# Kernel tuning notes

Measured on AMD Instinct MI355X. Metric: run time of the kernel, lower is better.

The kernel has to match this reference:

```python
import jax, jax.numpy as jnp
import numpy as np

N_NODES = 50000
N_EDGES = 800000
N_GRAPHS = 512
VOCAB = 128
HID = 64
NCLS = 5


def _seg_mean(vals, ids, num_segments):
    s = jax.ops.segment_sum(vals, ids, num_segments=num_segments)
    cnt = jax.ops.segment_sum(jnp.ones((vals.shape[0],), vals.dtype), ids, num_segments=num_segments)
    return s / jnp.maximum(cnt, 1.0)[:, None]


def sage_conv(x, src, dst, W_l, b_l, W_r):
    # PyG SAGEConv (mean aggr): out = lin_l(mean_{j in N(i)} x_j) + lin_r(x_i)
    agg = _seg_mean(x[src], dst, x.shape[0])          # [N, H] gather + scatter-mean
    return agg @ W_l.T + b_l + x @ W_r.T


def setup_inputs() -> dict:
    key = jax.random.key(0)
    ks = jax.random.split(key, 10)
    scale = 1.0 / np.sqrt(HID)
    x_tokens = jax.random.randint(ks[0], (N_NODES,), 0, VOCAB)
    edge_index = jax.random.randint(ks[1], (2, N_EDGES), 0, N_NODES)
    batch = jnp.sort(jax.random.randint(ks[2], (N_NODES,), 0, N_GRAPHS))
    return {
        "x_tokens": x_tokens,
        "edge_index": edge_index,
        "batch": batch,
        "embed": jax.random.normal(ks[3], (VOCAB, HID), jnp.float32),
        "W1l": jax.random.normal(ks[4], (HID, HID), jnp.float32) * scale,
        "b1l": jnp.zeros((HID,), jnp.float32),
        "W1r": jax.random.normal(ks[5], (HID, HID), jnp.float32) * scale,
        "W2l": jax.random.normal(ks[6], (HID, HID), jnp.float32) * scale,
        "b2l": jnp.zeros((HID,), jnp.float32),
        "W2r": jax.random.normal(ks[7], (HID, HID), jnp.float32) * scale,
        "Wlin": jax.random.normal(ks[8], (NCLS, HID), jnp.float32) * scale,
        "blin": jnp.zeros((NCLS,), jnp.float32),
    }


def reference(x_tokens, edge_index, batch, embed, W1l, b1l, W1r, W2l, b2l, W2r, Wlin, blin):
    src, dst = edge_index[0], edge_index[1]
    x = embed[x_tokens]                                  # [N, H] embedding lookup
    x = jax.nn.relu(sage_conv(x, src, dst, W1l, b1l, W1r))
    x = jax.nn.relu(sage_conv(x, src, dst, W2l, b2l, W2r))
    g = _seg_mean(x, batch, N_GRAPHS)                    # global_mean_pool -> [G, H]
    return g @ Wlin.T + blin                             # [G, num_classes]
```

## Files before the change

kernel.cpp:

```cpp
#include <hip/hip_runtime.h>

#define N_NODES  50000
#define N_EDGES  800000
#define N_GRAPHS 512
#define HID      64
#define NCLS     5
#define NB       64
#define EST      36

typedef __attribute__((ext_vector_type(8))) short bf16x8;
typedef __attribute__((ext_vector_type(4))) float f32x4;

__device__ inline unsigned short f2bf(float f) {
    unsigned int u = __builtin_bit_cast(unsigned int, f);
    unsigned int r = (u + 0x7FFFu + ((u >> 16) & 1u)) >> 16;
    return (unsigned short)r;
}
__device__ inline unsigned int packbf(float a, float b) {
    return (unsigned int)f2bf(a) | ((unsigned int)f2bf(b) << 16);
}
__device__ inline float bf2f(unsigned int u16) {
    unsigned int t = u16 << 16;
    return __builtin_bit_cast(float, t);
}

#define EBUF_T (128 * 32)
#define PW_T   (64 * 64)
#define PREP_T (EBUF_T + N_NODES + 2 * PW_T)
__global__ void k_prep(const float* __restrict__ embed, unsigned int* __restrict__ ebufg,
                       const int* __restrict__ batch,
                       int* __restrict__ pos_start, int* __restrict__ pos_end,
                       const float* __restrict__ W1l, const float* __restrict__ W1r,
                       unsigned int* __restrict__ wb1,
                       const float* __restrict__ W2l, const float* __restrict__ W2r,
                       unsigned int* __restrict__ wb2) {
    int gid = blockIdx.x * blockDim.x + threadIdx.x;
    if (gid < EBUF_T) {
        int t = gid >> 5, c = gid & 31;
        float2 v = ((const float2*)(embed + (long)t * HID))[c];
        ebufg[gid] = packbf(v.x, v.y);
        return;
    }
    gid -= EBUF_T;
    if (gid < N_NODES) {
        int n = gid;
        int b = batch[n];
        if (n == 0 || batch[n - 1] != b) pos_start[b] = n;
        if (n == N_NODES - 1 || batch[n + 1] != b) pos_end[b] = n + 1;
        return;
    }
    gid -= N_NODES;
    if (gid < 2 * PW_T) {
        const float* Wl = (gid < PW_T) ? W1l : W2l;
        const float* Wr = (gid < PW_T) ? W1r : W2r;
        unsigned int* wb = (gid < PW_T) ? wb1 : wb2;
        int i = (gid < PW_T) ? gid : gid - PW_T;
        int h = i >> 6, c = i & 63;
        float2 v = (c < 32) ? ((const float2*)(Wl + (long)h * HID))[c]
                            : ((const float2*)(Wr + (long)h * HID))[c - 32];
        wb[i] = packbf(v.x, v.y);
    }
}

__global__ void k_fill(const int* __restrict__ src, const int* __restrict__ dst,
                       const int* __restrict__ tok,
                       int* __restrict__ cnt, unsigned int* __restrict__ bucket) {
    int e = blockIdx.x * blockDim.x + threadIdx.x;
    if (e >= N_EDGES) return;
    int s = src[e], d = dst[e];
    unsigned int t = (unsigned int)tok[s];
    int pos = atomicAdd(&cnt[d], 1);
    if (pos < NB) bucket[(long)d * NB + pos] = (unsigned int)s | (t << 16);
}

__global__ __launch_bounds__(256) void k_agg1(
    const int* __restrict__ cnt, const unsigned int* __restrict__ bucket,
    const unsigned int* __restrict__ ebufg, unsigned int* __restrict__ aggb) {
    __shared__ unsigned int elds[128 * EST];
    const int tid = threadIdx.x;
    for (int i = tid; i < EBUF_T; i += 256) {
        int t = i >> 5, c = i & 31;
        elds[t * EST + c] = ebufg[i];
    }
    __syncthreads();

    int n    = (blockIdx.x * 256 + tid) >> 6;
    int lane = tid & 63;
    int q    = lane & 7;
    int e8   = lane >> 3;
    int deg  = cnt[n];
    int m    = min(deg, NB);
    unsigned int v = (lane < m) ? bucket[(long)n * NB + lane] : 0u;
    float f0 = 0, f1 = 0, f2 = 0, f3 = 0, f4 = 0, f5 = 0, f6 = 0, f7 = 0;
#pragma unroll
    for (int g = 0; g < 8; ++g) {
        int j = g * 8 + e8;
        unsigned int vv = __shfl(v, j, 64);
        if (j < m) {
            int tk = (int)(vv >> 16);
            uint4 w = *((const uint4*)(elds + tk * EST + q * 4));
            f0 += bf2f(w.x & 0xffff); f1 += bf2f(w.x >> 16);
            f2 += bf2f(w.y & 0xffff); f3 += bf2f(w.y >> 16);
            f4 += bf2f(w.z & 0xffff); f5 += bf2f(w.z >> 16);
            f6 += bf2f(w.w & 0xffff); f7 += bf2f(w.w >> 16);
        }
    }
#pragma unroll
    for (int o = 8; o < 64; o <<= 1) {
        f0 += __shfl_xor(f0, o, 64); f1 += __shfl_xor(f1, o, 64);
        f2 += __shfl_xor(f2, o, 64); f3 += __shfl_xor(f3, o, 64);
        f4 += __shfl_xor(f4, o, 64); f5 += __shfl_xor(f5, o, 64);
        f6 += __shfl_xor(f6, o, 64); f7 += __shfl_xor(f7, o, 64);
    }
    if (e8 == 0) {
        float inv = 1.0f / (float)max(deg, 1);
        uint4 o;
        o.x = packbf(f0 * inv, f1 * inv);
        o.y = packbf(f2 * inv, f3 * inv);
        o.z = packbf(f4 * inv, f5 * inv);
        o.w = packbf(f6 * inv, f7 * inv);
        *((uint4*)(aggb + (long)n * 32) + q) = o;
    }
}

__global__ __launch_bounds__(256) void k_agg2(
    const int* __restrict__ cnt, const unsigned int* __restrict__ bucket,
    const unsigned int* __restrict__ xb, unsigned int* __restrict__ aggb) {
    const int tid = threadIdx.x;
    int n    = (blockIdx.x * 256 + tid) >> 6;
    int lane = tid & 63;
    int q    = lane & 7;
    int e8   = lane >> 3;
    int deg  = cnt[n];
    int m    = min(deg, NB);
    unsigned int v = (lane < m) ? bucket[(long)n * NB + lane] : 0u;
    float f0 = 0, f1 = 0, f2 = 0, f3 = 0, f4 = 0, f5 = 0, f6 = 0, f7 = 0;
#pragma unroll
    for (int g = 0; g < 8; ++g) {
        int j = g * 8 + e8;
        unsigned int vv = __shfl(v, j, 64);
        if (j < m) {
            int s = (int)(vv & 0xffffu);
            uint4 w = *((const uint4*)(xb + (long)s * 32) + q);
            f0 += bf2f(w.x & 0xffff); f1 += bf2f(w.x >> 16);
            f2 += bf2f(w.y & 0xffff); f3 += bf2f(w.y >> 16);
            f4 += bf2f(w.z & 0xffff); f5 += bf2f(w.z >> 16);
            f6 += bf2f(w.w & 0xffff); f7 += bf2f(w.w >> 16);
        }
    }
#pragma unroll
    for (int o = 8; o < 64; o <<= 1) {
        f0 += __shfl_xor(f0, o, 64); f1 += __shfl_xor(f1, o, 64);
        f2 += __shfl_xor(f2, o, 64); f3 += __shfl_xor(f3, o, 64);
        f4 += __shfl_xor(f4, o, 64); f5 += __shfl_xor(f5, o, 64);
        f6 += __shfl_xor(f6, o, 64); f7 += __shfl_xor(f7, o, 64);
    }
    if (e8 == 0) {
        float inv = 1.0f / (float)max(deg, 1);
        uint4 o;
        o.x = packbf(f0 * inv, f1 * inv);
        o.y = packbf(f2 * inv, f3 * inv);
        o.z = packbf(f4 * inv, f5 * inv);
        o.w = packbf(f6 * inv, f7 * inv);
        *((uint4*)(aggb + (long)n * 32) + q) = o;
    }
}

__global__ __launch_bounds__(256) void k_transform(
    const unsigned int* __restrict__ aggb, const unsigned int* __restrict__ xsrc,
    const int* __restrict__ tok,
    const unsigned int* __restrict__ wb, const float* __restrict__ bl,
    unsigned short* __restrict__ xoutb)
{
    const int tid  = threadIdx.x;
    const int lane = tid & 63;
    const int w    = tid >> 6;
    const int nb   = blockIdx.x * 64 + w * 16;
    const int m    = lane & 15;
    const int quad = lane >> 4;

    int row  = nb + m;
    int rowc = min(row, N_NODES - 1);
    const unsigned int* selfp = tok ? (xsrc + (long)tok[rowc] * 32)
                                    : (xsrc + (long)rowc * 32);

    bf16x8 afr[4];
    afr[0] = *(const bf16x8*)(aggb + (long)rowc * 32 + quad * 4);
    afr[1] = *(const bf16x8*)(aggb + (long)rowc * 32 + 16 + quad * 4);
    afr[2] = *(const bf16x8*)(selfp + quad * 4);
    afr[3] = *(const bf16x8*)(selfp + 16 + quad * 4);

    f32x4 acc[4];
#pragma unroll
    for (int t = 0; t < 4; ++t) {
        acc[t] = (f32x4){0.f, 0.f, 0.f, 0.f};
#pragma unroll
        for (int kst = 0; kst < 4; ++kst) {
            bf16x8 bfr = *(const bf16x8*)(wb + (t * 16 + m) * 64 + kst * 16 + quad * 4);
            acc[t] = __builtin_amdgcn_mfma_f32_16x16x32_bf16(bfr, afr[kst], acc[t], 0, 0, 0);
        }
    }

    int node = nb + m;
    if (node < N_NODES) {
#pragma unroll
        for (int t = 0; t < 4; ++t) {
            int hb = t * 16 + quad * 4;
            float4 bb = *(const float4*)(bl + hb);
            ushort4 o;
            o.x = f2bf(fmaxf(acc[t][0] + bb.x, 0.f));
            o.y = f2bf(fmaxf(acc[t][1] + bb.y, 0.f));
            o.z = f2bf(fmaxf(acc[t][2] + bb.z, 0.f));
            o.w = f2bf(fmaxf(acc[t][3] + bb.w, 0.f));
            *(ushort4*)(xoutb + (long)node * HID + hb) = o;
        }
    }
}

__global__ __launch_bounds__(64) void k_pool(
    const unsigned int* __restrict__ x2b,
    const int* __restrict__ pos_start, const int* __restrict__ pos_end,
    const float* __restrict__ Wlin, const float* __restrict__ blin,
    float* __restrict__ out)
{
    int g    = blockIdx.x;
    int lane = threadIdx.x;
    int q    = lane & 7;
    int slot = lane >> 3;
    int s = pos_start[g], e = pos_end[g];
    float f0 = 0, f1 = 0, f2 = 0, f3 = 0, f4 = 0, f5 = 0, f6 = 0, f7 = 0;
    for (int n = s + slot; n < e; n += 8) {
        uint4 v = *((const uint4*)(x2b + (long)n * 32) + q);
        f0 += bf2f(v.x & 0xffff); f1 += bf2f(v.x >> 16);
        f2 += bf2f(v.y & 0xffff); f3 += bf2f(v.y >> 16);
        f4 += bf2f(v.z & 0xffff); f5 += bf2f(v.z >> 16);
        f6 += bf2f(v.w & 0xffff); f7 += bf2f(v.w >> 16);
    }
#pragma unroll
    for (int o = 8; o < 64; o <<= 1) {
        f0 += __shfl_xor(f0, o, 64); f1 += __shfl_xor(f1, o, 64);
        f2 += __shfl_xor(f2, o, 64); f3 += __shfl_xor(f3, o, 64);
        f4 += __shfl_xor(f4, o, 64); f5 += __shfl_xor(f5, o, 64);
        f6 += __shfl_xor(f6, o, 64); f7 += __shfl_xor(f7, o, 64);
    }
    float inv = 1.0f / (float)max(e - s, 1);
    f0 *= inv; f1 *= inv; f2 *= inv; f3 *= inv;
    f4 *= inv; f5 *= inv; f6 *= inv; f7 *= inv;
#pragma unroll
    for (int c = 0; c < NCLS; ++c) {
        const float* wr = Wlin + c * HID + q * 8;
        float p = f0 * wr[0] + f1 * wr[1] + f2 * wr[2] + f3 * wr[3] +
                  f4 * wr[4] + f5 * wr[5] + f6 * wr[6] + f7 * wr[7];
        p += __shfl_xor(p, 1, 64);
        p += __shfl_xor(p, 2, 64);
        p += __shfl_xor(p, 4, 64);
        if (lane == 0) out[g * NCLS + c] = p + blin[c];
    }
}

extern "C" void kernel_launch(void* const* d_in, const int* in_sizes, int n_in,
                              void* d_out, int out_size, void* d_ws, size_t ws_size,
                              hipStream_t stream) {
    const int*   tok   = (const int*)d_in[0];
    const int*   eidx  = (const int*)d_in[1];
    const int*   batch = (const int*)d_in[2];
    const float* embed = (const float*)d_in[3];
    const float* W1l   = (const float*)d_in[4];
    const float* b1l   = (const float*)d_in[5];
    const float* W1r   = (const float*)d_in[6];
    const float* W2l   = (const float*)d_in[7];
    const float* b2l   = (const float*)d_in[8];
    const float* W2r   = (const float*)d_in[9];
    const float* Wlin  = (const float*)d_in[10];
    const float* blin  = (const float*)d_in[11];
    float* out = (float*)d_out;

    const int* src = eidx;
    const int* dst = eidx + N_EDGES;

    char* wsp = (char*)d_ws;
    size_t off = 0;
    auto alloc = [&](size_t bytes) -> void* {
        void* p = wsp + off;
        off = (off + bytes + 255) & ~(size_t)255;
        return p;
    };
    int*   cnt     = (int*)  alloc((size_t)N_NODES * 4);
    int*   pstart  = (int*)  alloc((size_t)N_GRAPHS * 4);
    int*   pend    = (int*)  alloc((size_t)N_GRAPHS * 4);
    unsigned int* bucket = (unsigned int*)alloc((size_t)N_NODES * NB * 4);
    unsigned int* aggb   = (unsigned int*)alloc((size_t)N_NODES * 32 * 4);
    unsigned int* x1b    = (unsigned int*)alloc((size_t)N_NODES * 32 * 4);
    unsigned int* x2b    = (unsigned int*)alloc((size_t)N_NODES * 32 * 4);
    unsigned int* ebufg  = (unsigned int*)alloc((size_t)128 * 32 * 4);
    unsigned int* wb1    = (unsigned int*)alloc((size_t)64 * 64 * 4);
    unsigned int* wb2    = (unsigned int*)alloc((size_t)64 * 64 * 4);

    hipMemsetAsync(cnt, 0, (char*)pend - (char*)cnt + (size_t)N_GRAPHS * 4, stream);

    k_prep<<<(PREP_T + 255) / 256, 256, 0, stream>>>(
        embed, ebufg, batch, pstart, pend, W1l, W1r, wb1, W2l, W2r, wb2);

    k_fill<<<(N_EDGES + 255) / 256, 256, 0, stream>>>(src, dst, tok, cnt, bucket);

    const int ABLK = (N_NODES * 64) / 256;
    const int TBLK = (N_NODES + 63) / 64;
    k_agg1<<<ABLK, 256, 0, stream>>>(cnt, bucket, ebufg, aggb);
    k_transform<<<TBLK, 256, 0, stream>>>(aggb, ebufg, tok, wb1, b1l,
                                          (unsigned short*)x1b);
    k_agg2<<<ABLK, 256, 0, stream>>>(cnt, bucket, x1b, aggb);
    k_transform<<<TBLK, 256, 0, stream>>>(aggb, x1b, nullptr, wb2, b2l,
                                          (unsigned short*)x2b);

    k_pool<<<N_GRAPHS, 64, 0, stream>>>(x2b, pstart, pend, Wlin, blin, out);
}
```

Before: 212.6 us.

## Pre-pack edges in prep and partition bucket fill by destination residue

The token lookup and src/dst packing move into the prep kernel, which writes an 8-byte packed edge array. The fill kernel then launches 8 groups of blocks, each scanning all edges but handling only destinations whose index mod 8 matches the group. The aim is to localize atomic and scatter traffic into the per-node buckets and improve cache or XCD locality. In exchange, the edge array is read eight times, and an extra 6.4MB intermediate is written and read back.

```diff
diff --git a/kernel.cpp b/kernel.cpp
--- a/kernel.cpp
+++ b/kernel.cpp
@@ -7,6 +7,7 @@
 #define NCLS     5
 #define NB       64
 #define EST      36
+#define FILL_GB  128
 
 typedef __attribute__((ext_vector_type(8))) short bf16x8;
 typedef __attribute__((ext_vector_type(4))) float f32x4;
@@ -26,14 +27,17 @@
 
 #define EBUF_T (128 * 32)
 #define PW_T   (64 * 64)
-#define PREP_T (EBUF_T + N_NODES + 2 * PW_T)
-__global__ void k_prep(const float* __restrict__ embed, unsigned int* __restrict__ ebufg,
-                       const int* __restrict__ batch,
-                       int* __restrict__ pos_start, int* __restrict__ pos_end,
-                       const float* __restrict__ W1l, const float* __restrict__ W1r,
-                       unsigned int* __restrict__ wb1,
-                       const float* __restrict__ W2l, const float* __restrict__ W2r,
-                       unsigned int* __restrict__ wb2) {
+#define PREP_T (EBUF_T + N_NODES + 2 * PW_T + N_EDGES)
+__global__ void k_prep(
+    const float* __restrict__ embed, unsigned int* __restrict__ ebufg,
+    const int* __restrict__ batch,
+    int* __restrict__ pos_start, int* __restrict__ pos_end,
+    const float* __restrict__ W1l, const float* __restrict__ W1r,
+    unsigned int* __restrict__ wb1,
+    const float* __restrict__ W2l, const float* __restrict__ W2r,
+    unsigned int* __restrict__ wb2,
+    const int* __restrict__ src, const int* __restrict__ dst,
+    const int* __restrict__ tok, uint2* __restrict__ epack) {
     int gid = blockIdx.x * blockDim.x + threadIdx.x;
     if (gid < EBUF_T) {
         int t = gid >> 5, c = gid & 31;
@@ -59,18 +63,29 @@
         float2 v = (c < 32) ? ((const float2*)(Wl + (long)h * HID))[c]
                             : ((const float2*)(Wr + (long)h * HID))[c - 32];
         wb[i] = packbf(v.x, v.y);
-    }
-}
-
-__global__ void k_fill(const int* __restrict__ src, const int* __restrict__ dst,
-                       const int* __restrict__ tok,
-                       int* __restrict__ cnt, unsigned int* __restrict__ bucket) {
-    int e = blockIdx.x * blockDim.x + threadIdx.x;
-    if (e >= N_EDGES) return;
-    int s = src[e], d = dst[e];
-    unsigned int t = (unsigned int)tok[s];
-    int pos = atomicAdd(&cnt[d], 1);
-    if (pos < NB) bucket[(long)d * NB + pos] = (unsigned int)s | (t << 16);
+        return;
+    }
+    gid -= 2 * PW_T;
+    if (gid < N_EDGES) {
+        int s = src[gid];
+        unsigned int t = (unsigned int)tok[s];
+        epack[gid] = make_uint2((unsigned int)s | (t << 16), (unsigned int)dst[gid]);
+    }
+}
+
+__global__ __launch_bounds__(256) void k_fill(
+    const uint2* __restrict__ epack, int* __restrict__ cnt,
+    unsigned int* __restrict__ bucket) {
+    const int x  = blockIdx.x & 7;
+    const int bs = blockIdx.x >> 3;
+    for (int e = bs * 256 + threadIdx.x; e < N_EDGES; e += 256 * FILL_GB) {
+        uint2 v = epack[e];
+        int d = (int)v.y;
+        if ((d & 7) == x) {
+            int pos = atomicAdd(&cnt[d], 1);
+            if (pos < NB) bucket[(long)d * NB + pos] = v.x;
+        }
+    }
 }
 
 __global__ __launch_bounds__(256) void k_agg1(
@@ -289,6 +304,7 @@
     int*   pstart  = (int*)  alloc((size_t)N_GRAPHS * 4);
     int*   pend    = (int*)  alloc((size_t)N_GRAPHS * 4);
     unsigned int* bucket = (unsigned int*)alloc((size_t)N_NODES * NB * 4);
+    uint2* epack         = (uint2*)alloc((size_t)N_EDGES * 8);
     unsigned int* aggb   = (unsigned int*)alloc((size_t)N_NODES * 32 * 4);
     unsigned int* x1b    = (unsigned int*)alloc((size_t)N_NODES * 32 * 4);
     unsigned int* x2b    = (unsigned int*)alloc((size_t)N_NODES * 32 * 4);
@@ -299,9 +315,10 @@
     hipMemsetAsync(cnt, 0, (char*)pend - (char*)cnt + (size_t)N_GRAPHS * 4, stream);
 
     k_prep<<<(PREP_T + 255) / 256, 256, 0, stream>>>(
-        embed, ebufg, batch, pstart, pend, W1l, W1r, wb1, W2l, W2r, wb2);
-
-    k_fill<<<(N_EDGES + 255) / 256, 256, 0, stream>>>(src, dst, tok, cnt, bucket);
+        embed, ebufg, batch, pstart, pend, W1l, W1r, wb1, W2l, W2r, wb2,
+        src, dst, tok, epack);
+
+    k_fill<<<8 * FILL_GB, 256, 0, stream>>>(epack, cnt, bucket);
 
     const int ABLK = (N_NODES * 64) / 256;
     const int TBLK = (N_NODES + 63) / 64;
```

Result: no change. 215.8 us (+1.5%).

## Fuse neighbor aggregation and linear transform into one per-layer kernel

Applied to the files above, without the earlier changes.

Each SAGE layer now runs as a single kernel: 1024-thread blocks aggregate the neighbor means for 64 nodes into a shared-memory tile together with the self features, then run the MFMA transform straight from LDS. This removes the global aggb round-trip and two kernel launches. The cost is larger blocks that need a full-block barrier, and each wave does four nodes in sequence, which lowers occupancy and leaves less latency hiding for the gathers.

```diff
diff --git a/kernel.cpp b/kernel.cpp
--- a/kernel.cpp
+++ b/kernel.cpp
@@ -7,6 +7,7 @@
 #define NCLS     5
 #define NB       64
 #define EST      36
+#define AST      68
 
 typedef __attribute__((ext_vector_type(8))) short bf16x8;
 typedef __attribute__((ext_vector_type(4))) float f32x4;
@@ -27,13 +28,14 @@
 #define EBUF_T (128 * 32)
 #define PW_T   (64 * 64)
 #define PREP_T (EBUF_T + N_NODES + 2 * PW_T)
-__global__ void k_prep(const float* __restrict__ embed, unsigned int* __restrict__ ebufg,
-                       const int* __restrict__ batch,
-                       int* __restrict__ pos_start, int* __restrict__ pos_end,
-                       const float* __restrict__ W1l, const float* __restrict__ W1r,
-                       unsigned int* __restrict__ wb1,
-                       const float* __restrict__ W2l, const float* __restrict__ W2r,
-                       unsigned int* __restrict__ wb2) {
+__global__ void k_prep(
+    const float* __restrict__ embed, unsigned int* __restrict__ ebufg,
+    const int* __restrict__ batch,
+    int* __restrict__ pos_start, int* __restrict__ pos_end,
+    const float* __restrict__ W1l, const float* __restrict__ W1r,
+    unsigned int* __restrict__ wb1,
+    const float* __restrict__ W2l, const float* __restrict__ W2r,
+    unsigned int* __restrict__ wb2) {
     int gid = blockIdx.x * blockDim.x + threadIdx.x;
     if (gid < EBUF_T) {
         int t = gid >> 5, c = gid & 31;
@@ -73,147 +75,106 @@
     if (pos < NB) bucket[(long)d * NB + pos] = (unsigned int)s | (t << 16);
 }
 
-__global__ __launch_bounds__(256) void k_agg1(
+template <bool L1>
+__global__ __launch_bounds__(1024) void k_layer(
     const int* __restrict__ cnt, const unsigned int* __restrict__ bucket,
-    const unsigned int* __restrict__ ebufg, unsigned int* __restrict__ aggb) {
-    __shared__ unsigned int elds[128 * EST];
-    const int tid = threadIdx.x;
-    for (int i = tid; i < EBUF_T; i += 256) {
-        int t = i >> 5, c = i & 31;
-        elds[t * EST + c] = ebufg[i];
-    }
-    __syncthreads();
-
-    int n    = (blockIdx.x * 256 + tid) >> 6;
-    int lane = tid & 63;
-    int q    = lane & 7;
-    int e8   = lane >> 3;
-    int deg  = cnt[n];
-    int m    = min(deg, NB);
-    unsigned int v = (lane < m) ? bucket[(long)n * NB + lane] : 0u;
-    float f0 = 0, f1 = 0, f2 = 0, f3 = 0, f4 = 0, f5 = 0, f6 = 0, f7 = 0;
-#pragma unroll
-    for (int g = 0; g < 8; ++g) {
-        int j = g * 8 + e8;
-        unsigned int vv = __shfl(v, j, 64);
-        if (j < m) {
-            int tk = (int)(vv >> 16);
-            uint4 w = *((const uint4*)(elds + tk * EST + q * 4));
-            f0 += bf2f(w.x & 0xffff); f1 += bf2f(w.x >> 16);
-            f2 += bf2f(w.y & 0xffff); f3 += bf2f(w.y >> 16);
-            f4 += bf2f(w.z & 0xffff); f5 += bf2f(w.z >> 16);
-            f6 += bf2f(w.w & 0xffff); f7 += bf2f(w.w >> 16);
-        }
-    }
-#pragma unroll
-    for (int o = 8; o < 64; o <<= 1) {
-        f0 += __shfl_xor(f0, o, 64); f1 += __shfl_xor(f1, o, 64);
-        f2 += __shfl_xor(f2, o, 64); f3 += __shfl_xor(f3, o, 64);
-        f4 += __shfl_xor(f4, o, 64); f5 += __shfl_xor(f5, o, 64);
-        f6 += __shfl_xor(f6, o, 64); f7 += __shfl_xor(f7, o, 64);
-    }
-    if (e8 == 0) {
-        float inv = 1.0f / (float)max(deg, 1);
-        uint4 o;
-        o.x = packbf(f0 * inv, f1 * inv);
-        o.y = packbf(f2 * inv, f3 * inv);
-        o.z = packbf(f4 * inv, f5 * inv);
-        o.w = packbf(f6 * inv, f7 * inv);
-        *((uint4*)(aggb + (long)n * 32) + q) = o;
-    }
-}
-
-__global__ __launch_bounds__(256) void k_agg2(
-    const int* __restrict__ cnt, const unsigned int* __restrict__ bucket,
-    const unsigned int* __restrict__ xb, unsigned int* __restrict__ aggb) {
-    const int tid = threadIdx.x;
-    int n    = (blockIdx.x * 256 + tid) >> 6;
-    int lane = tid & 63;
-    int q    = lane & 7;
-    int e8   = lane >> 3;
-    int deg  = cnt[n];
-    int m    = min(deg, NB);
-    unsigned int v = (lane < m) ? bucket[(long)n * NB + lane] : 0u;
-    float f0 = 0, f1 = 0, f2 = 0, f3 = 0, f4 = 0, f5 = 0, f6 = 0, f7 = 0;
-#pragma unroll
-    for (int g = 0; g < 8; ++g) {
-        int j = g * 8 + e8;
-        unsigned int vv = __shfl(v, j, 64);
-        if (j < m) {
-            int s = (int)(vv & 0xffffu);
-            uint4 w = *((const uint4*)(xb + (long)s * 32) + q);
-            f0 += bf2f(w.x & 0xffff); f1 += bf2f(w.x >> 16);
-            f2 += bf2f(w.y & 0xffff); f3 += bf2f(w.y >> 16);
-            f4 += bf2f(w.z & 0xffff); f5 += bf2f(w.z >> 16);
-            f6 += bf2f(w.w & 0xffff); f7 += bf2f(w.w >> 16);
-        }
-    }
-#pragma unroll
-    for (int o = 8; o < 64; o <<= 1) {
-        f0 += __shfl_xor(f0, o, 64); f1 += __shfl_xor(f1, o, 64);
-        f2 += __shfl_xor(f2, o, 64); f3 += __shfl_xor(f3, o, 64);
-        f4 += __shfl_xor(f4, o, 64); f5 += __shfl_xor(f5, o, 64);
-        f6 += __shfl_xor(f6, o, 64); f7 += __shfl_xor(f7, o, 64);
-    }
-    if (e8 == 0) {
-        float inv = 1.0f / (float)max(deg, 1);
-        uint4 o;
-        o.x = packbf(f0 * inv, f1 * inv);
-        o.y = packbf(f2 * inv, f3 * inv);
-        o.z = packbf(f4 * inv, f5 * inv);
-        o.w = packbf(f6 * inv, f7 * inv);
-        *((uint4*)(aggb + (long)n * 32) + q) = o;
-    }
-}
-
-__global__ __launch_bounds__(256) void k_transform(
-    const unsigned int* __restrict__ aggb, const unsigned int* __restrict__ xsrc,
-    const int* __restrict__ tok,
+    const int* __restrict__ tok, const unsigned int* __restrict__ ebufg,
+    const unsigned int* __restrict__ xb,
     const unsigned int* __restrict__ wb, const float* __restrict__ bl,
     unsigned short* __restrict__ xoutb)
 {
+    __shared__ unsigned int As[64 * AST];
+    __shared__ unsigned int elds[L1 ? 128 * EST : 1];
     const int tid  = threadIdx.x;
+    const int wv   = tid >> 6;
     const int lane = tid & 63;
-    const int w    = tid >> 6;
-    const int nb   = blockIdx.x * 64 + w * 16;
-    const int m    = lane & 15;
+    const int n0   = blockIdx.x * 64;
+
+    if (L1) {
+        for (int i = tid; i < EBUF_T; i += 1024) {
+            int t = i >> 5, c = i & 31;
+            elds[t * EST + c] = ebufg[i];
+        }
+        __syncthreads();
+    }
+
+    const int q  = lane & 7;
+    const int e8 = lane >> 3;
+
+#pragma unroll
+    for (int i = 0; i < 4; ++i) {
+        int rl = wv * 4 + i;
+        int nn = n0 + rl;
+        int nc = min(nn, N_NODES - 1);
+        int deg = cnt[nc];
+        int m   = (nn < N_NODES) ? min(deg, NB) : 0;
+        unsigned int v = (lane < m) ? bucket[(long)nc * NB + lane] : 0u;
+        float f0 = 0, f1 = 0, f2 = 0, f3 = 0, f4 = 0, f5 = 0, f6 = 0, f7 = 0;
+#pragma unroll
+        for (int g = 0; g < 8; ++g) {
+            int j = g * 8 + e8;
+            unsigned int vv = __shfl(v, j, 64);
+            if (j < m) {
+                uint4 w4;
+                if (L1) w4 = *(const uint4*)(elds + (vv >> 16) * EST + q * 4);
+                else    w4 = *((const uint4*)(xb + (long)(vv & 0xffffu) * 32) + q);
+                f0 += bf2f(w4.x & 0xffff); f1 += bf2f(w4.x >> 16);
+                f2 += bf2f(w4.y & 0xffff); f3 += bf2f(w4.y >> 16);
+                f4 += bf2f(w4.z & 0xffff); f5 += bf2f(w4.z >> 16);
+                f6 += bf2f(w4.w & 0xffff); f7 += bf2f(w4.w >> 16);
+            }
+        }
+#pragma unroll
+        for (int o = 8; o < 64; o <<= 1) {
+            f0 += __shfl_xor(f0, o, 64); f1 += __shfl_xor(f1, o, 64);
+            f2 += __shfl_xor(f2, o, 64); f3 += __shfl_xor(f3, o, 64);
+            f4 += __shfl_xor(f4, o, 64); f5 += __shfl_xor(f5, o, 64);
+            f6 += __shfl_xor(f6, o, 64); f7 += __shfl_xor(f7, o, 64);
+        }
+        if (e8 == 0) {
+            float inv = 1.0f / (float)max(deg, 1);
+            uint4 o;
+            o.x = packbf(f0 * inv, f1 * inv);
+            o.y = packbf(f2 * inv, f3 * inv);
+            o.z = packbf(f4 * inv, f5 * inv);
+            o.w = packbf(f6 * inv, f7 * inv);
+            *(uint4*)(As + rl * AST + q * 4) = o;
+        } else if (e8 == 1) {
+            uint4 sv;
+            if (L1) { int tk = tok[nc]; sv = *(const uint4*)(elds + tk * EST + q * 4); }
+            else    { sv = *((const uint4*)(xb + (long)nc * 32) + q); }
+            *(uint4*)(As + rl * AST + 32 + q * 4) = sv;
+        }
+    }
+    __syncthreads();
+
+    const int s    = wv & 3;
+    const int t    = wv >> 2;
+    const int mm   = lane & 15;
     const int quad = lane >> 4;
 
-    int row  = nb + m;
-    int rowc = min(row, N_NODES - 1);
-    const unsigned int* selfp = tok ? (xsrc + (long)tok[rowc] * 32)
-                                    : (xsrc + (long)rowc * 32);
-
     bf16x8 afr[4];
-    afr[0] = *(const bf16x8*)(aggb + (long)rowc * 32 + quad * 4);
-    afr[1] = *(const bf16x8*)(aggb + (long)rowc * 32 + 16 + quad * 4);
-    afr[2] = *(const bf16x8*)(selfp + quad * 4);
-    afr[3] = *(const bf16x8*)(selfp + 16 + quad * 4);
-
-    f32x4 acc[4];
-#pragma unroll
-    for (int t = 0; t < 4; ++t) {
-        acc[t] = (f32x4){0.f, 0.f, 0.f, 0.f};
-#pragma unroll
-        for (int kst = 0; kst < 4; ++kst) {
-            bf16x8 bfr = *(const bf16x8*)(wb + (t * 16 + m) * 64 + kst * 16 + quad * 4);
-            acc[t] = __builtin_amdgcn_mfma_f32_16x16x32_bf16(bfr, afr[kst], acc[t], 0, 0, 0);
-        }
-    }
-
-    int node = nb + m;
+#pragma unroll
+    for (int kst = 0; kst < 4; ++kst)
+        afr[kst] = *(const bf16x8*)(As + (s * 16 + mm) * AST + kst * 16 + quad * 4);
+
+    f32x4 acc = (f32x4){0.f, 0.f, 0.f, 0.f};
+#pragma unroll
+    for (int kst = 0; kst < 4; ++kst) {
+        bf16x8 bfr = *(const bf16x8*)(wb + (t * 16 + mm) * 64 + kst * 16 + quad * 4);
+        acc = __builtin_amdgcn_mfma_f32_16x16x32_bf16(bfr, afr[kst], acc, 0, 0, 0);
+    }
+
+    int node = n0 + s * 16 + mm;
     if (node < N_NODES) {
-#pragma unroll
-        for (int t = 0; t < 4; ++t) {
-            int hb = t * 16 + quad * 4;
-            float4 bb = *(const float4*)(bl + hb);
-            ushort4 o;
-            o.x = f2bf(fmaxf(acc[t][0] + bb.x, 0.f));
-            o.y = f2bf(fmaxf(acc[t][1] + bb.y, 0.f));
-            o.z = f2bf(fmaxf(acc[t][2] + bb.z, 0.f));
-            o.w = f2bf(fmaxf(acc[t][3] + bb.w, 0.f));
-            *(ushort4*)(xoutb + (long)node * HID + hb) = o;
-        }
+        int hb = t * 16 + quad * 4;
+        float4 bb = *(const float4*)(bl + hb);
+        ushort4 o;
+        o.x = f2bf(fmaxf(acc[0] + bb.x, 0.f));
+        o.y = f2bf(fmaxf(acc[1] + bb.y, 0.f));
+        o.z = f2bf(fmaxf(acc[2] + bb.z, 0.f));
+        o.w = f2bf(fmaxf(acc[3] + bb.w, 0.f));
+        *(ushort4*)(xoutb + (long)node * HID + hb) = o;
     }
 }
 
@@ -289,7 +250,6 @@
     int*   pstart  = (int*)  alloc((size_t)N_GRAPHS * 4);
     int*   pend    = (int*)  alloc((size_t)N_GRAPHS * 4);
     unsigned int* bucket = (unsigned int*)alloc((size_t)N_NODES * NB * 4);
-    unsigned int* aggb   = (unsigned int*)alloc((size_t)N_NODES * 32 * 4);
     unsigned int* x1b    = (unsigned int*)alloc((size_t)N_NODES * 32 * 4);
     unsigned int* x2b    = (unsigned int*)alloc((size_t)N_NODES * 32 * 4);
     unsigned int* ebufg  = (unsigned int*)alloc((size_t)128 * 32 * 4);
@@ -303,14 +263,11 @@
 
     k_fill<<<(N_EDGES + 255) / 256, 256, 0, stream>>>(src, dst, tok, cnt, bucket);
 
-    const int ABLK = (N_NODES * 64) / 256;
-    const int TBLK = (N_NODES + 63) / 64;
-    k_agg1<<<ABLK, 256, 0, stream>>>(cnt, bucket, ebufg, aggb);
-    k_transform<<<TBLK, 256, 0, stream>>>(aggb, ebufg, tok, wb1, b1l,
-                                          (unsigned short*)x1b);
-    k_agg2<<<ABLK, 256, 0, stream>>>(cnt, bucket, x1b, aggb);
-    k_transform<<<TBLK, 256, 0, stream>>>(aggb, x1b, nullptr, wb2, b2l,
-                                          (unsigned short*)x2b);
+    const int LBLK = (N_NODES + 63) / 64;
+    k_layer<true><<<LBLK, 1024, 0, stream>>>(cnt, bucket, tok, ebufg, nullptr,
+                                             wb1, b1l, (unsigned short*)x1b);
+    k_layer<false><<<LBLK, 1024, 0, stream>>>(cnt, bucket, nullptr, nullptr, x1b,
+                                              wb2, b2l, (unsigned short*)x2b);
 
     k_pool<<<N_GRAPHS, 64, 0, stream>>>(x2b, pstart, pend, Wlin, blin, out);
 }
```

Measured after the change: 208.6 us. Within noise of the previous version (-1.9%).
